# Kernel optimization log

Measured on AMD Instinct MI355X. Metric: run time of the kernel, lower is better.

The kernel has to match this reference:

```python
import jax, jax.numpy as jnp
import numpy as np

# Complete binary tree: B trees, L leaves each, processed level-synchronously.
B, L, IN_DIM, MEM = 64, 1024, 300, 256


def setup_inputs() -> dict:
    key = jax.random.key(0)
    ks = jax.random.split(key, 6)
    s = 0.05
    embs = jax.random.normal(ks[0], (B, L, IN_DIM), dtype=jnp.float32)
    # Leaf module: c = cx(x); h = sigmoid(ox(x)) * tanh(c)
    Wcx = jax.random.normal(ks[1], (MEM, IN_DIM), dtype=jnp.float32) * s
    bcx = jnp.zeros((MEM,), jnp.float32)
    Wox = jax.random.normal(ks[2], (MEM, IN_DIM), dtype=jnp.float32) * s
    box = jnp.zeros((MEM,), jnp.float32)
    # Composer: 4 gates (i, lf, rf, u), each gate = Linear(lh) + Linear(rh).
    # Stacked: Wl/Wr have shape [4, MEM, MEM]; biases [4, MEM].
    Wl = jax.random.normal(ks[3], (4, MEM, MEM), dtype=jnp.float32) * s
    bl = jnp.zeros((4, MEM), jnp.float32)
    Wr = jax.random.normal(ks[4], (4, MEM, MEM), dtype=jnp.float32) * s
    br = jnp.zeros((4, MEM), jnp.float32)
    return dict(embs=embs, Wcx=Wcx, bcx=bcx, Wox=Wox, box=box,
                Wl=Wl, bl=bl, Wr=Wr, br=br)


def reference(embs, Wcx, bcx, Wox, box, Wl, bl, Wr, br):
    # Leaf module (BinaryTreeLeafModule.forward), vectorized over all leaves.
    c = jnp.einsum('blx,mx->blm', embs, Wcx) + bcx          # [B, L, MEM]
    o = jax.nn.sigmoid(jnp.einsum('blx,mx->blm', embs, Wox) + box)
    h = o * jnp.tanh(c)

    bias = bl + br                                          # [4, MEM]
    n = c.shape[1]
    while n > 1:  # log2(L) levels, static unrolled loop
        lc, rc = c[:, 0::2], c[:, 1::2]                     # [B, n/2, MEM]
        lh, rh = h[:, 0::2], h[:, 1::2]
        # All 4 gate pre-activations fused: [B, n/2, 4, MEM]
        g = (jnp.einsum('bnm,gom->bngo', lh, Wl)
             + jnp.einsum('bnm,gom->bngo', rh, Wr) + bias)
        i = jax.nn.sigmoid(g[..., 0, :])
        lf = jax.nn.sigmoid(g[..., 1, :])
        rf = jax.nn.sigmoid(g[..., 2, :])
        u = jnp.tanh(g[..., 3, :])
        c = i * u + lf * lc + rf * rc                       # composer cell
        h = jnp.tanh(c)                                     # gate_output=False path
        n //= 2

    # Root state (tree.state = (c, h)); stacked as [2, B, MEM]
    return jnp.stack([c[:, 0], h[:, 0]])
```

## Files before the change

### kernel.cpp

```cpp
#include <hip/hip_runtime.h>
#include <hip/hip_bf16.h>
#include <hip/hip_fp16.h>


typedef __attribute__((ext_vector_type(8))) short bf16x8;
typedef __attribute__((ext_vector_type(4))) float f32x4;

__device__ __forceinline__ float fsig(float x)  { return 1.f / (1.f + __expf(-x)); }
__device__ __forceinline__ float ftanh(float x) { return 1.f - 2.f / (__expf(2.f * x) + 1.f); }
__device__ __forceinline__ ushort f2bf(float x) {
    __hip_bfloat16 b = __float2bfloat16(x);
    return *reinterpret_cast<ushort*>(&b);
}

__device__ __forceinline__ void gld_lds16(const void* g, void* l) {
    __builtin_amdgcn_global_load_lds((const __attribute__((address_space(1))) void*)g,
                                     (__attribute__((address_space(3))) void*)l, 16, 0, 0);
}

__global__ void prep(const float* __restrict__ Wl,  const float* __restrict__ Wr,
                     const float* __restrict__ bl,  const float* __restrict__ br,
                     const float* __restrict__ Wcx, const float* __restrict__ Wox,
                     const float* __restrict__ bcx, const float* __restrict__ box,
                     const float* __restrict__ embs,
                     ushort* __restrict__ Wb2, ushort* __restrict__ WbL,
                     float* __restrict__ bp2, float* __restrict__ bpL,
                     ushort* __restrict__ embsB)
{
    const int gid = blockIdx.x * 256 + threadIdx.x;
    for (int i = gid; i < 524288; i += 262144) {
        int e = i & 7, slot = (i >> 3) & 3, o = (i >> 5) & 255;
        int g = (i >> 13) & 3, t = i >> 15;
        int q = slot ^ ((o >> 1) & 3);
        int k = t * 32 + q * 8 + e;
        float v = (k < 256) ? Wl[(g * 256 + o) * 256 + k]
                            : Wr[(g * 256 + o) * 256 + (k - 256)];
        Wb2[i] = f2bf(v);
    }
    if (gid < 163840) {
        int e = gid & 7, slot = (gid >> 3) & 3, o = (gid >> 5) & 255;
        int g = (gid >> 13) & 1, t = gid >> 14;
        int q = slot ^ ((o >> 1) & 3);
        int k = t * 32 + q * 8 + e;
        float v = 0.f;
        if (k < 300) v = g ? Wox[o * 300 + k] : Wcx[o * 300 + k];
        WbL[gid] = f2bf(v);
    }
    if (gid < 1024) bp2[gid] = bl[gid] + br[gid];
    if (gid < 512) {
        int g = gid >> 8, o = gid & 255;
        bpL[gid] = g ? box[o] : bcx[o];
    }
    for (int i = gid; i < 65536 * 80; i += 262144) {
        int row = i / 80;
        int k = (i - row * 80) * 4;
        float4 v = make_float4(0.f, 0.f, 0.f, 0.f);
        if (k < 300) v = *(const float4*)(embs + (size_t)row * 300 + k);
        ushort4 o4;
        o4.x = f2bf(v.x); o4.y = f2bf(v.y); o4.z = f2bf(v.z); o4.w = f2bf(v.w);
        *(ushort4*)(embsB + (size_t)row * 320 + k) = o4;
    }
}

template<int NG, int HALVES, int MODE>
__global__ __launch_bounds__(256, 4)
void mfma_gemm(const ushort* __restrict__ A,
               const ushort* __restrict__ Wb,
               const float* __restrict__ bp,
               const __half* __restrict__ Cprev,
               __half* __restrict__ c_out,
               ushort* __restrict__ h_out,
               int M)
{
    constexpr int K = HALVES * 32;
    constexpr int OW = 128 / NG;
    __shared__ __align__(16) ushort As[2][512 * 8];
    __shared__ __align__(16) ushort Bs[2][512 * 8];

    const int tid = threadIdx.x;
    const int wid = tid >> 6, ln = tid & 63;
    const int lq = ln >> 4, lr = ln & 15;
    const int wm = wid >> 1, wn = wid & 1;
    const int rowBlk = blockIdx.x * 128;
    const int o0 = blockIdx.y * OW;

    f32x4 acc[4][4];
#pragma unroll
    for (int m = 0; m < 4; ++m)
#pragma unroll
        for (int f = 0; f < 4; ++f) acc[m][f] = f32x4{0.f, 0.f, 0.f, 0.f};

    const int ar0 = tid >> 2,  as0 = tid & 3;
    const int ar1 = ar0 + 64;
    const int aq0 = (as0 - ((ar0 >> 1) & 3)) & 3;
    const int aq1 = (as0 - ((ar1 >> 1) & 3)) & 3;
    const ushort* aP0 = A + (size_t)min(rowBlk + ar0, M - 1) * K + aq0 * 8;
    const ushort* aP1 = A + (size_t)min(rowBlk + ar1, M - 1) * K + aq1 * 8;
    const int bj0 = tid >> 2,        bs0 = tid & 3;
    const int bj1 = (tid + 256) >> 2;
    const int bg0 = bj0 / OW, bo0 = o0 + (bj0 & (OW - 1));
    const int bg1 = bj1 / OW, bo1 = o0 + (bj1 & (OW - 1));
    const ushort* bP0 = Wb + ((size_t)bg0 * 1024 + bo0 * 4 + bs0) * 8;
    const ushort* bP1 = Wb + ((size_t)bg1 * 1024 + bo1 * 4 + bs0) * 8;
    constexpr size_t BSTR = (size_t)NG * 1024 * 8;

    const int aSw = (lq + ((lr >> 1) & 3)) & 3;
    const int bSw = lq ^ ((lr >> 1) & 3);
    int aOff[4];
#pragma unroll
    for (int m = 0; m < 4; ++m)
        aOff[m] = ((wm * 64 + m * 16 + lr) * 4 + aSw) * 8;
    int bOff[4];
#pragma unroll
    for (int f = 0; f < 4; ++f)
        bOff[f] = ((f * 32 + wn * 16 + lr) * 4 + bSw) * 8;

    gld_lds16(aP0, &As[0][tid * 8]);
    gld_lds16(aP1, &As[0][(tid + 256) * 8]);
    gld_lds16(bP0, &Bs[0][tid * 8]);
    gld_lds16(bP1, &Bs[0][(tid + 256) * 8]);

#pragma unroll
    for (int h = 0; h < HALVES; ++h) {
        __syncthreads();
        const int cur = h & 1;
        if (h + 1 < HALVES) {
            gld_lds16(aP0 + (size_t)(h + 1) * 32, &As[cur ^ 1][tid * 8]);
            gld_lds16(aP1 + (size_t)(h + 1) * 32, &As[cur ^ 1][(tid + 256) * 8]);
            gld_lds16(bP0 + (size_t)(h + 1) * BSTR, &Bs[cur ^ 1][tid * 8]);
            gld_lds16(bP1 + (size_t)(h + 1) * BSTR, &Bs[cur ^ 1][(tid + 256) * 8]);
        }
        bf16x8 a[4];
#pragma unroll
        for (int m = 0; m < 4; ++m)
            a[m] = *(const bf16x8*)&As[cur][aOff[m]];
#pragma unroll
        for (int f = 0; f < 4; ++f) {
            bf16x8 b = *(const bf16x8*)&Bs[cur][bOff[f]];
#pragma unroll
            for (int m = 0; m < 4; ++m)
                acc[m][f] = __builtin_amdgcn_mfma_f32_16x16x32_bf16(a[m], b, acc[m][f], 0, 0, 0);
        }
    }

#pragma unroll
    for (int m = 0; m < 4; ++m) {
        const int row0 = rowBlk + wm * 64 + m * 16 + lq * 4;
        if constexpr (MODE == 0) {
#pragma unroll
            for (int ob = 0; ob < 2; ++ob) {
                const int col = o0 + ob * 32 + wn * 16 + lr;
                const float bc = bp[col], bo = bp[256 + col];
#pragma unroll
                for (int j = 0; j < 4; ++j) {
                    int row = row0 + j;
                    if (row < M) {
                        float cv = acc[m][ob][j] + bc;
                        float ov = acc[m][2 + ob][j] + bo;
                        c_out[(size_t)row * 256 + col] = __float2half(cv);
                        h_out[(size_t)row * 256 + col] = f2bf(fsig(ov) * ftanh(cv));
                    }
                }
            }
        } else {
            const int col = o0 + wn * 16 + lr;
            const float bi  = bp[col],       blf = bp[256 + col];
            const float brf = bp[512 + col], bu  = bp[768 + col];
#pragma unroll
            for (int j = 0; j < 4; ++j) {
                int row = row0 + j;
                if (row < M) {
                    float gi = fsig(acc[m][0][j] + bi);
                    float lf = fsig(acc[m][1][j] + blf);
                    float rf = fsig(acc[m][2][j] + brf);
                    float gu = ftanh(acc[m][3][j] + bu);
                    float lc = __half2float(Cprev[(size_t)row * 512 + col]);
                    float rc = __half2float(Cprev[(size_t)row * 512 + 256 + col]);
                    float cv = gi * gu + lf * lc + rf * rc;
                    c_out[(size_t)row * 256 + col] = __float2half(cv);
                    h_out[(size_t)row * 256 + col] = f2bf(ftanh(cv));
                }
            }
        }
    }
}

__global__ __launch_bounds__(512, 1)
void tail_lstm(const ushort* __restrict__ hin,
               const __half* __restrict__ cin,
               const ushort* __restrict__ Wb,
               const float* __restrict__ bp,
               float* __restrict__ dout)
{
    __shared__ __align__(16) ushort HA[32 * 256];
    __shared__ __align__(16) float  CA[32 * 256];
    __shared__ __align__(16) ushort HB[16 * 256];
    __shared__ __align__(16) float  CB[16 * 256];

    const int b = blockIdx.x;
    const int tid = threadIdx.x;
    const int wid = tid >> 6, ln = tid & 63;
    const int lq = ln >> 4, lr = ln & 15;

    int o_[2], sl_[2];
    const ushort* bB[2];
#pragma unroll
    for (int of = 0; of < 2; ++of) {
        o_[of] = wid * 32 + of * 16 + lr;
        sl_[of] = lq ^ ((o_[of] >> 1) & 3);
        bB[of] = Wb + (size_t)(o_[of] * 4 + sl_[of]) * 8;
    }
    const float bi0  = bp[o_[0]],       blf0 = bp[256 + o_[0]];
    const float brf0 = bp[512 + o_[0]], bu0  = bp[768 + o_[0]];
    const float bi1  = bp[o_[1]],       blf1 = bp[256 + o_[1]];
    const float brf1 = bp[512 + o_[1]], bu1  = bp[768 + o_[1]];

    {
        const ushort* hbase = hin + (size_t)b * 64 * 256;
        f32x4 acc[2][2][4];
#pragma unroll
        for (int m = 0; m < 2; ++m)
#pragma unroll
            for (int of = 0; of < 2; ++of)
#pragma unroll
                for (int g = 0; g < 4; ++g) acc[m][of][g] = f32x4{0.f, 0.f, 0.f, 0.f};

        bf16x8 b0[2][4], b1[2][4], a0[2], a1[2];
#pragma unroll
        for (int of = 0; of < 2; ++of)
#pragma unroll
            for (int g = 0; g < 4; ++g)
                b0[of][g] = *(const bf16x8*)(bB[of] + (size_t)g * 8192);
#pragma unroll
        for (int m = 0; m < 2; ++m) {
            int pr = 32 * m + 2 * lr;
            a0[m] = *(const bf16x8*)(hbase + (size_t)pr * 256 + lq * 8);
        }

#pragma unroll 1
        for (int ks = 0; ks < 16; ks += 2) {
            if (ks + 1 < 16) {
#pragma unroll
                for (int of = 0; of < 2; ++of)
#pragma unroll
                    for (int g = 0; g < 4; ++g)
                        b1[of][g] = *(const bf16x8*)(bB[of] + (size_t)((ks + 1) * 4 + g) * 8192);
#pragma unroll
                for (int m = 0; m < 2; ++m) {
                    int pr = 32 * m + 2 * lr + ((ks + 1) >> 3);
                    int pc = lq + ((ks + 1) & 7) * 4;
                    a1[m] = *(const bf16x8*)(hbase + (size_t)pr * 256 + pc * 8);
                }
            }
#pragma unroll
            for (int m = 0; m < 2; ++m)
#pragma unroll
                for (int of = 0; of < 2; ++of)
#pragma unroll
                    for (int g = 0; g < 4; ++g)
                        acc[m][of][g] = __builtin_amdgcn_mfma_f32_16x16x32_bf16(a0[m], b0[of][g], acc[m][of][g], 0, 0, 0);
            if (ks + 2 < 16) {
#pragma unroll
                for (int of = 0; of < 2; ++of)
#pragma unroll
                    for (int g = 0; g < 4; ++g)
                        b0[of][g] = *(const bf16x8*)(bB[of] + (size_t)((ks + 2) * 4 + g) * 8192);
#pragma unroll
                for (int m = 0; m < 2; ++m) {
                    int pr = 32 * m + 2 * lr + ((ks + 2) >> 3);
                    int pc = lq + ((ks + 2) & 7) * 4;
                    a0[m] = *(const bf16x8*)(hbase + (size_t)pr * 256 + pc * 8);
                }
            }
#pragma unroll
            for (int m = 0; m < 2; ++m)
#pragma unroll
                for (int of = 0; of < 2; ++of)
#pragma unroll
                    for (int g = 0; g < 4; ++g)
                        acc[m][of][g] = __builtin_amdgcn_mfma_f32_16x16x32_bf16(a1[m], b1[of][g], acc[m][of][g], 0, 0, 0);
        }

        const __half* cbase = cin + (size_t)b * 64 * 256;
#pragma unroll
        for (int m = 0; m < 2; ++m)
#pragma unroll
        for (int of = 0; of < 2; ++of) {
            const int col = o_[of];
            const float vbi  = of ? bi1 : bi0,   vblf = of ? blf1 : blf0;
            const float vbrf = of ? brf1 : brf0, vbu  = of ? bu1 : bu0;
#pragma unroll
            for (int j = 0; j < 4; ++j) {
                int row = m * 16 + lq * 4 + j;
                float gi = fsig(acc[m][of][0][j] + vbi);
                float lf = fsig(acc[m][of][1][j] + vblf);
                float rf = fsig(acc[m][of][2][j] + vbrf);
                float gu = ftanh(acc[m][of][3][j] + vbu);
                float lc = __half2float(cbase[(size_t)(2 * row) * 256 + col]);
                float rc = __half2float(cbase[(size_t)(2 * row + 1) * 256 + col]);
                float cv = gi * gu + lf * lc + rf * rc;
                float hv = ftanh(cv);
                CA[row * 256 + col] = cv;
                HA[row * 256 + (((col >> 3) ^ ((row >> 1) & 7)) * 8) + (col & 7)] = f2bf(hv);
            }
        }
        __syncthreads();
    }

#pragma unroll 1
    for (int lvl = 1; lvl < 6; ++lvl) {
        const int npo = 32 >> lvl;
        const ushort* Hin = (lvl & 1) ? HA : HB;
        ushort*       Hout = (lvl & 1) ? HB : HA;
        const float*  Cin = (lvl & 1) ? CA : CB;
        float*        Cout = (lvl & 1) ? CB : CA;

        f32x4 acc[2][4];
#pragma unroll
        for (int of = 0; of < 2; ++of)
#pragma unroll
            for (int g = 0; g < 4; ++g) acc[of][g] = f32x4{0.f, 0.f, 0.f, 0.f};

        bf16x8 b0[2][4], b1[2][4], a0, a1;
#pragma unroll
        for (int of = 0; of < 2; ++of)
#pragma unroll
            for (int g = 0; g < 4; ++g)
                b0[of][g] = *(const bf16x8*)(bB[of] + (size_t)g * 8192);
        {
            int pr = 2 * lr;
            a0 = *(const bf16x8*)&Hin[pr * 256 + ((lq ^ ((pr >> 1) & 7)) * 8)];
        }

#pragma unroll 1
        for (int ks = 0; ks < 16; ks += 2) {
            if (ks + 1 < 16) {
#pragma unroll
                for (int of = 0; of < 2; ++of)
#pragma unroll
                    for (int g = 0; g < 4; ++g)
                        b1[of][g] = *(const bf16x8*)(bB[of] + (size_t)((ks + 1) * 4 + g) * 8192);
                int pr = 2 * lr + ((ks + 1) >> 3), pc = lq + ((ks + 1) & 7) * 4;
                a1 = *(const bf16x8*)&Hin[pr * 256 + ((pc ^ ((pr >> 1) & 7)) * 8)];
            }
#pragma unroll
            for (int of = 0; of < 2; ++of)
#pragma unroll
                for (int g = 0; g < 4; ++g)
                    acc[of][g] = __builtin_amdgcn_mfma_f32_16x16x32_bf16(a0, b0[of][g], acc[of][g], 0, 0, 0);
            if (ks + 2 < 16) {
#pragma unroll
                for (int of = 0; of < 2; ++of)
#pragma unroll
                    for (int g = 0; g < 4; ++g)
                        b0[of][g] = *(const bf16x8*)(bB[of] + (size_t)((ks + 2) * 4 + g) * 8192);
                int pr = 2 * lr + ((ks + 2) >> 3), pc = lq + ((ks + 2) & 7) * 4;
                a0 = *(const bf16x8*)&Hin[pr * 256 + ((pc ^ ((pr >> 1) & 7)) * 8)];
            }
#pragma unroll
            for (int of = 0; of < 2; ++of)
#pragma unroll
                for (int g = 0; g < 4; ++g)
                    acc[of][g] = __builtin_amdgcn_mfma_f32_16x16x32_bf16(a1, b1[of][g], acc[of][g], 0, 0, 0);
        }

#pragma unroll
        for (int of = 0; of < 2; ++of) {
            const int col = o_[of];
            const float vbi  = of ? bi1 : bi0,   vblf = of ? blf1 : blf0;
            const float vbrf = of ? brf1 : brf0, vbu  = of ? bu1 : bu0;
#pragma unroll
            for (int j = 0; j < 4; ++j) {
                int row = lq * 4 + j;
                if (row < npo) {
                    float gi = fsig(acc[of][0][j] + vbi);
                    float lf = fsig(acc[of][1][j] + vblf);
                    float rf = fsig(acc[of][2][j] + vbrf);
                    float gu = ftanh(acc[of][3][j] + vbu);
                    float lc = Cin[(2 * row) * 256 + col];
                    float rc = Cin[(2 * row + 1) * 256 + col];
                    float cv = gi * gu + lf * lc + rf * rc;
                    float hv = ftanh(cv);
                    if (lvl == 5) {
                        dout[b * 256 + col] = cv;
                        dout[16384 + b * 256 + col] = hv;
                    } else {
                        Cout[row * 256 + col] = cv;
                        Hout[row * 256 + (((col >> 3) ^ ((row >> 1) & 7)) * 8) + (col & 7)] = f2bf(hv);
                    }
                }
            }
        }
        __syncthreads();
    }
}


extern "C" void kernel_launch(void* const* d_in, const int* in_sizes, int n_in,
                              void* d_out, int out_size, void* d_ws, size_t ws_size,
                              hipStream_t stream)
{
    const float* embs = (const float*)d_in[0];
    const float* Wcx  = (const float*)d_in[1];
    const float* bcx  = (const float*)d_in[2];
    const float* Wox  = (const float*)d_in[3];
    const float* box  = (const float*)d_in[4];
    const float* Wl   = (const float*)d_in[5];
    const float* bl   = (const float*)d_in[6];
    const float* Wr   = (const float*)d_in[7];
    const float* br   = (const float*)d_in[8];

    char* p = (char*)d_ws;
    ushort* Wb2 = (ushort*)p;  p += (size_t)524288 * 2;
    ushort* WbL = (ushort*)p;  p += (size_t)163840 * 2;
    float*  bp2 = (float*)p;   p += 1024 * 4;
    float*  bpL = (float*)p;   p += 512 * 4;
    __half* c0  = (__half*)p;  p += (size_t)65536 * 256 * 2;
    ushort* h0  = (ushort*)p;  p += (size_t)65536 * 256 * 2;
    char* X = p;
    ushort* embsB = (ushort*)X;
    __half* cA = (__half*)X;
    ushort* hA = (ushort*)(X + (size_t)16 * 1024 * 1024);
    __half* cB = (__half*)(X + (size_t)32 * 1024 * 1024);
    ushort* hB = (ushort*)(X + (size_t)40 * 1024 * 1024);

    prep<<<1024, 256, 0, stream>>>(Wl, Wr, bl, br, Wcx, Wox, bcx, box, embs,
                                   Wb2, WbL, bp2, bpL, embsB);

    mfma_gemm<2, 10, 0><<<dim3(512, 4), 256, 0, stream>>>(
        embsB, WbL, bpL, nullptr, c0, h0, 65536);

    mfma_gemm<4, 16, 1><<<dim3(256, 8), 256, 0, stream>>>(
        h0, Wb2, bp2, c0, cA, hA, 32768);
    mfma_gemm<4, 16, 1><<<dim3(128, 8), 256, 0, stream>>>(
        hA, Wb2, bp2, cA, cB, hB, 16384);
    mfma_gemm<4, 16, 1><<<dim3(64, 8), 256, 0, stream>>>(
        hB, Wb2, bp2, cB, cA, hA, 8192);
    mfma_gemm<4, 16, 1><<<dim3(32, 8), 256, 0, stream>>>(
        hA, Wb2, bp2, cA, cB, hB, 4096);

    tail_lstm<<<64, 512, 0, stream>>>(
        hB, cB, Wb2, bp2, (float*)d_out);
}
```

Measured before the change: 256.6 us.

## Fuse fp32-to-bf16 embedding conversion into the leaf GEMM A-tile staging

Removes the separate pass in prep that converted the fp32 embeddings into a padded bf16 buffer. The leaf GEMM now reads the fp32 rows directly, converts them in registers and stores the bf16 values into LDS, zero-padding past column 300. This avoids writing and re-reading a 40MB intermediate. The cost is that A-tile loads become synchronous register loads instead of async global_load_lds. Each block also reads twice as many bytes for A, and the prefetch now stalls on the load latency inside the loop.

```diff
diff --git a/kernel.cpp b/kernel.cpp
--- a/kernel.cpp
+++ b/kernel.cpp
@@ -18,14 +18,25 @@
                                      (__attribute__((address_space(3))) void*)l, 16, 0, 0);
 }
 
+__device__ __forceinline__ void stageA_f32(const float* rowp, int kbase, ushort* dst)
+{
+    float4 x0 = make_float4(0.f, 0.f, 0.f, 0.f), x1 = x0;
+    if (kbase <= 296) x0 = *(const float4*)(rowp + kbase);
+    if (kbase <= 288) x1 = *(const float4*)(rowp + kbase + 4);
+    bf16x8 r;
+    r[0] = (short)f2bf(x0.x); r[1] = (short)f2bf(x0.y);
+    r[2] = (short)f2bf(x0.z); r[3] = (short)f2bf(x0.w);
+    r[4] = (short)f2bf(x1.x); r[5] = (short)f2bf(x1.y);
+    r[6] = (short)f2bf(x1.z); r[7] = (short)f2bf(x1.w);
+    *(bf16x8*)dst = r;
+}
+
 __global__ void prep(const float* __restrict__ Wl,  const float* __restrict__ Wr,
                      const float* __restrict__ bl,  const float* __restrict__ br,
                      const float* __restrict__ Wcx, const float* __restrict__ Wox,
                      const float* __restrict__ bcx, const float* __restrict__ box,
-                     const float* __restrict__ embs,
                      ushort* __restrict__ Wb2, ushort* __restrict__ WbL,
-                     float* __restrict__ bp2, float* __restrict__ bpL,
-                     ushort* __restrict__ embsB)
+                     float* __restrict__ bp2, float* __restrict__ bpL)
 {
     const int gid = blockIdx.x * 256 + threadIdx.x;
     for (int i = gid; i < 524288; i += 262144) {
@@ -51,20 +62,13 @@
         int g = gid >> 8, o = gid & 255;
         bpL[gid] = g ? box[o] : bcx[o];
     }
-    for (int i = gid; i < 65536 * 80; i += 262144) {
-        int row = i / 80;
-        int k = (i - row * 80) * 4;
-        float4 v = make_float4(0.f, 0.f, 0.f, 0.f);
-        if (k < 300) v = *(const float4*)(embs + (size_t)row * 300 + k);
-        ushort4 o4;
-        o4.x = f2bf(v.x); o4.y = f2bf(v.y); o4.z = f2bf(v.z); o4.w = f2bf(v.w);
-        *(ushort4*)(embsB + (size_t)row * 320 + k) = o4;
-    }
-}
+}
+
 
 template<int NG, int HALVES, int MODE>
 __global__ __launch_bounds__(256, 4)
 void mfma_gemm(const ushort* __restrict__ A,
+               const float* __restrict__ Af,
                const ushort* __restrict__ Wb,
                const float* __restrict__ bp,
                const __half* __restrict__ Cprev,
@@ -94,8 +98,15 @@
     const int ar1 = ar0 + 64;
     const int aq0 = (as0 - ((ar0 >> 1) & 3)) & 3;
     const int aq1 = (as0 - ((ar1 >> 1) & 3)) & 3;
-    const ushort* aP0 = A + (size_t)min(rowBlk + ar0, M - 1) * K + aq0 * 8;
-    const ushort* aP1 = A + (size_t)min(rowBlk + ar1, M - 1) * K + aq1 * 8;
+    const ushort* aP0 = nullptr; const ushort* aP1 = nullptr;
+    const float* fP0 = nullptr; const float* fP1 = nullptr;
+    if constexpr (MODE == 0) {
+        fP0 = Af + (size_t)min(rowBlk + ar0, M - 1) * 300;
+        fP1 = Af + (size_t)min(rowBlk + ar1, M - 1) * 300;
+    } else {
+        aP0 = A + (size_t)min(rowBlk + ar0, M - 1) * K + aq0 * 8;
+        aP1 = A + (size_t)min(rowBlk + ar1, M - 1) * K + aq1 * 8;
+    }
     const int bj0 = tid >> 2,        bs0 = tid & 3;
     const int bj1 = (tid + 256) >> 2;
     const int bg0 = bj0 / OW, bo0 = o0 + (bj0 & (OW - 1));
@@ -115,8 +126,13 @@
     for (int f = 0; f < 4; ++f)
         bOff[f] = ((f * 32 + wn * 16 + lr) * 4 + bSw) * 8;
 
-    gld_lds16(aP0, &As[0][tid * 8]);
-    gld_lds16(aP1, &As[0][(tid + 256) * 8]);
+    if constexpr (MODE == 0) {
+        stageA_f32(fP0, aq0 * 8, &As[0][tid * 8]);
+        stageA_f32(fP1, aq1 * 8, &As[0][(tid + 256) * 8]);
+    } else {
+        gld_lds16(aP0, &As[0][tid * 8]);
+        gld_lds16(aP1, &As[0][(tid + 256) * 8]);
+    }
     gld_lds16(bP0, &Bs[0][tid * 8]);
     gld_lds16(bP1, &Bs[0][(tid + 256) * 8]);
 
@@ -125,8 +141,13 @@
         __syncthreads();
         const int cur = h & 1;
         if (h + 1 < HALVES) {
-            gld_lds16(aP0 + (size_t)(h + 1) * 32, &As[cur ^ 1][tid * 8]);
-            gld_lds16(aP1 + (size_t)(h + 1) * 32, &As[cur ^ 1][(tid + 256) * 8]);
+            if constexpr (MODE == 0) {
+                stageA_f32(fP0, (h + 1) * 32 + aq0 * 8, &As[cur ^ 1][tid * 8]);
+                stageA_f32(fP1, (h + 1) * 32 + aq1 * 8, &As[cur ^ 1][(tid + 256) * 8]);
+            } else {
+                gld_lds16(aP0 + (size_t)(h + 1) * 32, &As[cur ^ 1][tid * 8]);
+                gld_lds16(aP1 + (size_t)(h + 1) * 32, &As[cur ^ 1][(tid + 256) * 8]);
+            }
             gld_lds16(bP0 + (size_t)(h + 1) * BSTR, &Bs[cur ^ 1][tid * 8]);
             gld_lds16(bP1 + (size_t)(h + 1) * BSTR, &Bs[cur ^ 1][(tid + 256) * 8]);
         }
@@ -418,26 +439,25 @@
     __half* c0  = (__half*)p;  p += (size_t)65536 * 256 * 2;
     ushort* h0  = (ushort*)p;  p += (size_t)65536 * 256 * 2;
     char* X = p;
-    ushort* embsB = (ushort*)X;
     __half* cA = (__half*)X;
     ushort* hA = (ushort*)(X + (size_t)16 * 1024 * 1024);
     __half* cB = (__half*)(X + (size_t)32 * 1024 * 1024);
     ushort* hB = (ushort*)(X + (size_t)40 * 1024 * 1024);
 
-    prep<<<1024, 256, 0, stream>>>(Wl, Wr, bl, br, Wcx, Wox, bcx, box, embs,
-                                   Wb2, WbL, bp2, bpL, embsB);
+    prep<<<1024, 256, 0, stream>>>(Wl, Wr, bl, br, Wcx, Wox, bcx, box,
+                                   Wb2, WbL, bp2, bpL);
 
     mfma_gemm<2, 10, 0><<<dim3(512, 4), 256, 0, stream>>>(
-        embsB, WbL, bpL, nullptr, c0, h0, 65536);
+        nullptr, embs, WbL, bpL, nullptr, c0, h0, 65536);
 
     mfma_gemm<4, 16, 1><<<dim3(256, 8), 256, 0, stream>>>(
-        h0, Wb2, bp2, c0, cA, hA, 32768);
+        h0, nullptr, Wb2, bp2, c0, cA, hA, 32768);
     mfma_gemm<4, 16, 1><<<dim3(128, 8), 256, 0, stream>>>(
-        hA, Wb2, bp2, cA, cB, hB, 16384);
+        hA, nullptr, Wb2, bp2, cA, cB, hB, 16384);
     mfma_gemm<4, 16, 1><<<dim3(64, 8), 256, 0, stream>>>(
-        hB, Wb2, bp2, cB, cA, hA, 8192);
+        hB, nullptr, Wb2, bp2, cB, cA, hA, 8192);
     mfma_gemm<4, 16, 1><<<dim3(32, 8), 256, 0, stream>>>(
-        hA, Wb2, bp2, cA, cB, hB, 4096);
+        hA, nullptr, Wb2, bp2, cA, cB, hB, 4096);
 
     tail_lstm<<<64, 512, 0, stream>>>(
         hB, cB, Wb2, bp2, (float*)d_out);
```

New measurement: 276.2 us. +7.6%, slower.
